# Performance work log

Measured on AMD Instinct MI355X. Metric: run time of the kernel, lower is better.

## Reference

```python
import jax, jax.numpy as jnp
import numpy as np

PRIME = 2147483647  # 2^31 - 1, MinHash modulus
GAMMA = 0.3
NUM_HEADS = 8


def minhash_sketch(ids, a, b):
    # ids: (B, L, S) int64 atom ids; a,b: (K,) hash coefficients
    # h[b,l,s,k] = (a[k]*id + b[k]) mod PRIME ; signature = min over the set axis S
    h = (ids[..., None] * a + b) % PRIME          # (B, L, S, K)
    return h.min(axis=2)                          # (B, L, K)


def jaccard_from_signatures(sig_q, sig_k):
    # sig_q: (B, Lq, K), sig_k: (B, Lk, K) -> (B, Lq, Lk) fraction of matching slots.
    # Scan over the K hash slots to avoid materializing a (B,Lq,Lk,K) tensor.
    B, Lq, K = sig_q.shape
    Lk = sig_k.shape[1]

    def step(acc, cols):
        qc, kc = cols                              # (B,Lq), (B,Lk)
        return acc + (qc[:, :, None] == kc[:, None, :]).astype(jnp.float32), None

    init = jnp.zeros((B, Lq, Lk), jnp.float32)
    xs = (jnp.moveaxis(sig_q, -1, 0), jnp.moveaxis(sig_k, -1, 0))
    acc, _ = jax.lax.scan(step, init, xs)
    return acc / K


def symdiff_from_jaccard(jacc, size_q, size_k):
    # |A ∩ B| = J/(1+J) * (|A|+|B|)  =>  |A Δ B| = (|A|+|B|) * (1-J)/(1+J)
    tot = size_q[:, :, None] + size_k[:, None, :]   # (B, Lq, Lk)
    return tot * (1.0 - jacc) / (1.0 + jacc)


def setup_inputs() -> dict:
    key = jax.random.key(0)
    ks = jax.random.split(key, 12)
    B, Lq, Lk, E, S, K, V = 4, 1024, 1024, 512, 8, 128, 32000
    w = lambda k: (jax.random.normal(k, (E, E), jnp.float32) * 0.02)
    return {
        "query": jax.random.normal(ks[0], (B, Lq, E), jnp.float32),
        "key": jax.random.normal(ks[1], (B, Lk, E), jnp.float32),
        "value": jax.random.normal(ks[2], (B, Lk, E), jnp.float32),
        "token_sets_q": jax.random.randint(ks[3], (B, Lq, S), 0, V).astype(jnp.int64),
        "token_sets_k": jax.random.randint(ks[4], (B, Lk, S), 0, V).astype(jnp.int64),
        "hash_a": jax.random.randint(ks[5], (K,), 1, PRIME - 1).astype(jnp.int64),
        "hash_b": jax.random.randint(ks[6], (K,), 0, PRIME - 1).astype(jnp.int64),
        "Wq": w(ks[7]), "bq": jnp.zeros((E,), jnp.float32),
        "Wk": w(ks[8]), "bk": jnp.zeros((E,), jnp.float32),
        "Wv": w(ks[9]), "bv": jnp.zeros((E,), jnp.float32),
        "Wo": w(ks[10]), "bo": jnp.zeros((E,), jnp.float32),
    }


def reference(query, key, value, token_sets_q, token_sets_k, hash_a, hash_b,
              Wq, bq, Wk, bk, Wv, bv, Wo, bo):
    B, Lq, E = query.shape
    Lk = key.shape[1]
    H = NUM_HEADS
    d = E // H

    # in-projections (torch Linear: x @ W^T + b); q,k are computed but the
    # attention scores come solely from the token-set kernel (gating disabled)
    q = query @ Wq.T + bq
    k = key @ Wk.T + bk
    v = (value @ Wv.T + bv).reshape(B, Lk, H, d).transpose(0, 2, 1, 3)  # (B,H,Lk,d)

    # MinHash sketches of per-token atom sets -> estimated Jaccard -> Δ-RBF score
    sig_q = minhash_sketch(token_sets_q, hash_a, hash_b)   # (B,Lq,K)
    sig_k = minhash_sketch(token_sets_k, hash_a, hash_b)   # (B,Lk,K)
    jacc = jaccard_from_signatures(sig_q, sig_k)           # (B,Lq,Lk)

    S = token_sets_q.shape[-1]
    size_q = jnp.full((B, Lq), S, jnp.float32)             # uniform CSR offsets -> |set| = S
    size_k = jnp.full((B, Lk), S, jnp.float32)
    delta = symdiff_from_jaccard(jacc, size_q, size_k)
    scores = jnp.exp(-GAMMA * delta)                       # (B,Lq,Lk), shared by all heads

    attn = jax.nn.softmax(scores, axis=-1)                 # no masks, no causal, dropout=0
    ctx = jnp.einsum('bqk,bhkd->bqhd', attn, v).reshape(B, Lq, E)
    return ctx @ Wo.T + bo
```

## Files before the change

kernel.cpp:

```cpp
#include <hip/hip_runtime.h>
#include <hip/hip_bf16.h>
#include <stdint.h>

#define PRIME 2147483647u
#define GAMMA 0.3f
#define K_HASH 128
#define S_SET 8
#define NB 4
#define LQ 1024
#define LK 1024
#define EDIM 512

typedef unsigned short ushort_t;
typedef __attribute__((ext_vector_type(8))) short short8;
typedef __attribute__((ext_vector_type(4))) float f32x4;

static __device__ __forceinline__ unsigned short f2bf(float f) {
    unsigned u = __builtin_bit_cast(unsigned, f);
    u += 0x7FFFu + ((u >> 16) & 1u);
    return (unsigned short)(u >> 16);
}

static __device__ __forceinline__ void glds16(const void* g, void* l) {
    __builtin_amdgcn_global_load_lds(
        (const __attribute__((address_space(1))) unsigned int*)g,
        (__attribute__((address_space(3))) unsigned int*)l, 16, 0, 0);
}

#define SWZ(r) ((((r) >> 2) & 3) ^ ((r) & 3))

static __device__ __forceinline__ unsigned nm2(unsigned acc, unsigned a,
                                               unsigned b, unsigned ones) {
    unsigned x = a ^ b, t;
    asm("v_pk_min_u16 %0, %1, %2" : "=v"(t) : "v"(x), "v"(ones));
    return acc + t;
}
static __device__ __forceinline__ unsigned nm8(unsigned acc, int4 q, int4 k,
                                               unsigned ones) {
    acc = nm2(acc, (unsigned)q.x, (unsigned)k.x, ones);
    acc = nm2(acc, (unsigned)q.y, (unsigned)k.y, ones);
    acc = nm2(acc, (unsigned)q.z, (unsigned)k.z, ones);
    acc = nm2(acc, (unsigned)q.w, (unsigned)k.w, ones);
    return acc;
}

#define CVT_N0 (NB * LK * EDIM)
#define CVT_N1 (EDIM * EDIM)
#define CVT_N2 (EDIM * EDIM)
#define CVT_BLOCKS ((CVT_N0 + CVT_N1 + CVT_N2) / (256 * 8))
#define SIG_BLOCKS (NB * (LQ + LK) / 2)

__global__ __launch_bounds__(256) void prep_kernel(
        const float* __restrict__ v, const float* __restrict__ wv,
        const float* __restrict__ wo,
        ushort_t* __restrict__ vb, ushort_t* __restrict__ wvb,
        ushort_t* __restrict__ wob,
        const int* __restrict__ ts_q, const int* __restrict__ ts_k,
        const int* __restrict__ ha, const int* __restrict__ hb,
        ushort_t* __restrict__ sig_q, ushort_t* __restrict__ sig_k,
        float* __restrict__ rs) {
    int blk = blockIdx.x;
    if (blk < CVT_BLOCKS) {
        size_t i = ((size_t)blk * 256 + threadIdx.x) * 8;
        const float* src; ushort_t* dst; size_t off;
        if (i < CVT_N0)                { src = v;  dst = vb;  off = i; }
        else if (i < CVT_N0 + CVT_N1)  { src = wv; dst = wvb; off = i - CVT_N0; }
        else                           { src = wo; dst = wob; off = i - CVT_N0 - CVT_N1; }
        float4 a = *(const float4*)(src + off);
        float4 b = *(const float4*)(src + off + 4);
        ushort4 o0, o1;
        o0.x = f2bf(a.x); o0.y = f2bf(a.y); o0.z = f2bf(a.z); o0.w = f2bf(a.w);
        o1.x = f2bf(b.x); o1.y = f2bf(b.y); o1.z = f2bf(b.z); o1.w = f2bf(b.w);
        *(ushort4*)(dst + off)     = o0;
        *(ushort4*)(dst + off + 4) = o1;
        return;
    }
    int sb = blk - CVT_BLOCKS;
    if (sb < 16) rs[sb * 256 + threadIdx.x] = 0.f;
    int half = threadIdx.x >> 7, k = threadIdx.x & 127;
    int row = sb * 2 + half;
    const int* ts = (row < NB * LQ) ? ts_q : ts_k;
    ushort_t* sig = (row < NB * LQ) ? sig_q : sig_k;
    int idx = row & (NB * LQ - 1);
    unsigned long long a  = (unsigned)ha[k];
    unsigned long long bb = (unsigned)hb[k];
    __shared__ int ids[2][S_SET];
    if (k < S_SET) ids[half][k] = ts[idx * S_SET + k];
    __syncthreads();
    unsigned mn = 0xFFFFFFFFu;
    #pragma unroll
    for (int s = 0; s < S_SET; s++) {
        unsigned long long x = a * (unsigned long long)(unsigned)ids[half][s] + bb;
        x = (x & PRIME) + (x >> 31);
        x = (x & PRIME) + (x >> 31);
        unsigned r = (unsigned)x;
        if (r >= PRIME) r -= PRIME;
        mn = (r < mn) ? r : mn;
    }
    sig[idx * K_HASH + k] = (ushort_t)mn;
}

__global__ __launch_bounds__(256) void jaccard_kernel(
        const ushort_t* __restrict__ sig_q, const ushort_t* __restrict__ sig_k,
        ushort_t* __restrict__ P, float* __restrict__ rs) {
    __shared__ int Qs[4][128 * 16];
    __shared__ int Ks[4][64 * 17];
    __shared__ float lut[K_HASH + 1];
    int tid = threadIdx.x;
    if (tid <= K_HASH) {
        float r = (float)(K_HASH - tid) / (float)(K_HASH + tid);
        lut[tid] = expf(expf(-GAMMA * (2.0f * S_SET) * r));
    }
    int b = blockIdx.z;
    int q0 = blockIdx.y * 128, j0 = blockIdx.x * 64;
    const int4* gq = (const int4*)(sig_q + ((size_t)b * LQ + q0) * K_HASH);
    const int4* gk = (const int4*)(sig_k + ((size_t)b * LK + j0) * K_HASH);
    int r0 = tid >> 2, g0 = tid & 3;
    int r1 = 64 + r0;
    #pragma unroll
    for (int ch = 0; ch < 4; ch++) {
        *(int4*)&Qs[ch][r0 * 16 + ((g0 + (r0 >> 3)) & 3) * 4] = gq[r0 * 16 + ch * 4 + g0];
        *(int4*)&Qs[ch][r1 * 16 + ((g0 + (r1 >> 3)) & 3) * 4] = gq[r1 * 16 + ch * 4 + g0];
        *(int4*)&Ks[ch][r0 * 17 + ((g0 + (r0 >> 5)) & 3) * 4] = gk[r0 * 16 + ch * 4 + g0];
    }
    __syncthreads();
    int tx = tid & 15, ty = tid >> 4;
    unsigned ones = 0x00010001u;
    unsigned acc[8][4] = {};

    auto ldq = [&](int ch, int cc, int4* qd) {
        #pragma unroll
        for (int i = 0; i < 8; i++)
            qd[i] = *(const int4*)&Qs[ch][(ty * 8 + i) * 16 + ((cc + ty) & 3) * 4];
    };
    auto ldk = [&](int ch, int cc, int4* kd) {
        #pragma unroll
        for (int j = 0; j < 4; j++)
            kd[j] = *(const int4*)&Ks[ch][(tx * 4 + j) * 17 + ((cc + (tx >> 3)) & 3) * 4];
    };

    int4 qa[8], ka[4], qb[8], kb[4];
    ldq(0, 0, qa); ldk(0, 0, ka);
    #pragma unroll 1
    for (int ch = 0; ch < 4; ch++) {
        #pragma unroll
        for (int cc = 0; cc < 4; cc++) {
            int nch = (cc == 3) ? ((ch + 1) & 3) : ch;
            int ncc = (cc + 1) & 3;
            ldq(nch, ncc, qb); ldk(nch, ncc, kb);
            #pragma unroll
            for (int i = 0; i < 8; i++)
                #pragma unroll
                for (int j = 0; j < 4; j++)
                    acc[i][j] = nm8(acc[i][j], qa[i], ka[j], ones);
            #pragma unroll
            for (int i = 0; i < 8; i++) qa[i] = qb[i];
            #pragma unroll
            for (int j = 0; j < 4; j++) ka[j] = kb[j];
        }
    }
    ushort_t* Pb = P + (size_t)b * LQ * LK;
    float fsum[8];
    #pragma unroll
    for (int i = 0; i < 8; i++) {
        ushort4 o;
        unsigned nm0 = (acc[i][0] & 0xFFFFu) + (acc[i][0] >> 16);
        unsigned nm1 = (acc[i][1] & 0xFFFFu) + (acc[i][1] >> 16);
        unsigned nm2_ = (acc[i][2] & 0xFFFFu) + (acc[i][2] >> 16);
        unsigned nm3 = (acc[i][3] & 0xFFFFu) + (acc[i][3] >> 16);
        float p0 = lut[K_HASH - nm0], p1 = lut[K_HASH - nm1];
        float p2 = lut[K_HASH - nm2_], p3 = lut[K_HASH - nm3];
        fsum[i] = (p0 + p1) + (p2 + p3);
        o.x = f2bf(p0); o.y = f2bf(p1); o.z = f2bf(p2); o.w = f2bf(p3);
        int row = q0 + ty * 8 + i;
        *(ushort4*)&Pb[(size_t)row * LK + j0 + tx * 4] = o;
    }
    __syncthreads();
    float* fs = (float*)&Qs[0][0];
    #pragma unroll
    for (int i = 0; i < 8; i++) fs[(ty * 8 + i) * 16 + tx] = fsum[i];
    __syncthreads();
    if (tid < 128) {
        float s = 0.f;
        #pragma unroll
        for (int t = 0; t < 16; t++) s += fs[tid * 16 + t];
        atomicAdd(&rs[(size_t)b * LQ + q0 + tid], s);
    }
}

#define EPI_ROWBIAS  0
#define EPI_ROWDIV   1
#define EPI_COLBIAS  2

template<int OUTF32, int MODE>
__global__ __launch_bounds__(256) void btgemm_kernel(
        const ushort_t* __restrict__ A, const ushort_t* __restrict__ B,
        void* __restrict__ C,
        const float* __restrict__ bias, const float* __restrict__ scale,
        int lda, int ldb, int ldc, int Kd,
        long long sA, long long sB, long long sC, long long sS) {
    __shared__ ushort_t As[2][64 * 32];
    __shared__ ushort_t Bs[2][64 * 32];
    int z = blockIdx.z;
    int m0 = blockIdx.y * 64, n0 = blockIdx.x * 64;
    int tid = threadIdx.x;
    int w = tid >> 6, lane = tid & 63;
    int wm = (w & 1) * 32, wn = (w >> 1) * 32;
    int mrow = lane & 15, kg = lane >> 4;

    int r = tid >> 2, c = (tid & 3) ^ SWZ(r);
    const ushort_t* pa = A + (size_t)z * sA + (size_t)(m0 + r) * lda + c * 8;
    const ushort_t* pb = B + (size_t)z * sB + (size_t)(n0 + r) * ldb + c * 8;

    int aoff[2], boff[2];
    #pragma unroll
    for (int s = 0; s < 2; s++) {
        int Ra = wm + s * 16 + mrow;
        aoff[s] = Ra * 32 + (kg ^ SWZ(Ra)) * 8;
        int Rb = wn + s * 16 + mrow;
        boff[s] = Rb * 32 + (kg ^ SWZ(Rb)) * 8;
    }

    f32x4 acc[2][2] = {};
    int nK = Kd >> 5;
    glds16(pa, &As[0][tid * 8]);
    glds16(pb, &Bs[0][tid * 8]);
    for (int i = 0; i < nK; i++) {
        __syncthreads();
        int cur = i & 1, nxt = cur ^ 1;
        if (i + 1 < nK) {
            int k0 = (i + 1) << 5;
            glds16(pa + k0, &As[nxt][tid * 8]);
            glds16(pb + k0, &Bs[nxt][tid * 8]);
        }
        short8 af[2], bh[2];
        #pragma unroll
        for (int s = 0; s < 2; s++) {
            af[s] = *(const short8*)&As[cur][aoff[s]];
            bh[s] = *(const short8*)&Bs[cur][boff[s]];
        }
        #pragma unroll
        for (int ii = 0; ii < 2; ii++)
            #pragma unroll
            for (int jj = 0; jj < 2; jj++)
                acc[ii][jj] = __builtin_amdgcn_mfma_f32_16x16x32_bf16(
                                  af[ii], bh[jj], acc[ii][jj], 0, 0, 0);
    }

    const float* sc = scale + (size_t)z * sS;
    int col = lane & 15, rbase = (lane >> 4) * 4;
    #pragma unroll
    for (int ii = 0; ii < 2; ii++) {
        #pragma unroll
        for (int jj = 0; jj < 2; jj++) {
            #pragma unroll
            for (int rr = 0; rr < 4; rr++) {
                int gm = m0 + wm + ii * 16 + rbase + rr;
                int gn = n0 + wn + jj * 16 + col;
                float v = acc[ii][jj][rr];
                if (MODE == EPI_ROWBIAS)     v += bias[gm];
                else if (MODE == EPI_ROWDIV) v /= sc[gm];
                else                         v += bias[gn];
                size_t cix = (size_t)z * sC + (size_t)gm * ldc + gn;
                if (OUTF32) ((float*)C)[cix] = v;
                else        ((ushort_t*)C)[cix] = f2bf(v);
            }
        }
    }
}

extern "C" void kernel_launch(void* const* d_in, const int* in_sizes, int n_in,
                              void* d_out, int out_size, void* d_ws, size_t ws_size,
                              hipStream_t stream) {
    const float* value = (const float*)d_in[2];
    const int* tsq = (const int*)d_in[3];
    const int* tsk = (const int*)d_in[4];
    const int* ha  = (const int*)d_in[5];
    const int* hb  = (const int*)d_in[6];
    const float* Wv = (const float*)d_in[11];
    const float* bv = (const float*)d_in[12];
    const float* Wo = (const float*)d_in[13];
    const float* bo = (const float*)d_in[14];
    float* out = (float*)d_out;

    char* ws = (char*)d_ws;
    ushort_t* sigq   = (ushort_t*)(ws);
    ushort_t* sigk   = (ushort_t*)(ws + (1ull << 20));
    ushort_t* P      = (ushort_t*)(ws + (4ull << 20));
    float* rs        = (float*)(ws + (12ull << 20));
    ushort_t* Vt     = (ushort_t*)(ws + (12ull << 20) + (1ull << 16));
    ushort_t* ctx    = (ushort_t*)(ws + (17ull << 20));
    ushort_t* Vb     = (ushort_t*)(ws + (21ull << 20));
    ushort_t* Wvb    = (ushort_t*)(ws + (25ull << 20));
    ushort_t* Wob    = (ushort_t*)(ws + (25ull << 20) + (512ull << 10));

    prep_kernel<<<CVT_BLOCKS + SIG_BLOCKS, 256, 0, stream>>>(
        value, Wv, Wo, Vb, Wvb, Wob, tsq, tsk, ha, hb, sigq, sigk, rs);

    jaccard_kernel<<<dim3(LK / 64, LQ / 128, NB), 256, 0, stream>>>(sigq, sigk, P, rs);

    btgemm_kernel<0, EPI_ROWBIAS><<<dim3(4096 / 64, 512 / 64, 1), 256, 0, stream>>>(
        Wvb, Vb, Vt, bv, rs ,
        EDIM, EDIM, NB * LK, EDIM, 0LL, 0LL, 0LL, 0LL);

    btgemm_kernel<0, EPI_ROWDIV><<<dim3(EDIM / 64, LQ / 64, NB), 256, 0, stream>>>(
        P, Vt, ctx, bv , rs,
        LK, NB * LK, EDIM, LK,
        (long long)LQ * LK, (long long)LK, (long long)LQ * EDIM, (long long)LQ);

    btgemm_kernel<1, EPI_COLBIAS><<<dim3(EDIM / 64, NB * LQ / 64, 1), 256, 0, stream>>>(
        ctx, Wob, out, bo, rs ,
        EDIM, EDIM, EDIM, EDIM, 0LL, 0LL, 0LL, 0LL);
}
```

Measured before the change: 156.6 us.

## Shrink Jaccard tile to 64x64 and stage signatures in two halves

The Jaccard kernel's output tile drops from 128x64 to 64x64, so each thread accumulates 4x4 instead of 8x4 counts and the grid doubles. The signature slots are now loaded into shared memory in two halves with an XOR-swizzled, padded layout, replacing the full preload and the register double-buffered LDS reads. This cuts shared memory and register use to raise occupancy and block count, at the cost of less reuse per loaded signature, extra barriers, and no software prefetch overlap.

New measurement: 154.8 us. No clear change (-1.1%).

```diff
diff --git a/kernel.cpp b/kernel.cpp
--- a/kernel.cpp
+++ b/kernel.cpp
@@ -103,8 +103,8 @@
 __global__ __launch_bounds__(256) void jaccard_kernel(
         const ushort_t* __restrict__ sig_q, const ushort_t* __restrict__ sig_k,
         ushort_t* __restrict__ P, float* __restrict__ rs) {
-    __shared__ int Qs[4][128 * 16];
-    __shared__ int Ks[4][64 * 17];
+    __shared__ int Qs[64 * 36];
+    __shared__ int Ks[64 * 36];
     __shared__ float lut[K_HASH + 1];
     int tid = threadIdx.x;
     if (tid <= K_HASH) {
@@ -112,75 +112,62 @@
         lut[tid] = expf(expf(-GAMMA * (2.0f * S_SET) * r));
     }
     int b = blockIdx.z;
-    int q0 = blockIdx.y * 128, j0 = blockIdx.x * 64;
+    int q0 = blockIdx.y * 64, j0 = blockIdx.x * 64;
     const int4* gq = (const int4*)(sig_q + ((size_t)b * LQ + q0) * K_HASH);
     const int4* gk = (const int4*)(sig_k + ((size_t)b * LK + j0) * K_HASH);
-    int r0 = tid >> 2, g0 = tid & 3;
-    int r1 = 64 + r0;
-    #pragma unroll
-    for (int ch = 0; ch < 4; ch++) {
-        *(int4*)&Qs[ch][r0 * 16 + ((g0 + (r0 >> 3)) & 3) * 4] = gq[r0 * 16 + ch * 4 + g0];
-        *(int4*)&Qs[ch][r1 * 16 + ((g0 + (r1 >> 3)) & 3) * 4] = gq[r1 * 16 + ch * 4 + g0];
-        *(int4*)&Ks[ch][r0 * 17 + ((g0 + (r0 >> 5)) & 3) * 4] = gk[r0 * 16 + ch * 4 + g0];
-    }
-    __syncthreads();
     int tx = tid & 15, ty = tid >> 4;
     unsigned ones = 0x00010001u;
-    unsigned acc[8][4] = {};
-
-    auto ldq = [&](int ch, int cc, int4* qd) {
-        #pragma unroll
-        for (int i = 0; i < 8; i++)
-            qd[i] = *(const int4*)&Qs[ch][(ty * 8 + i) * 16 + ((cc + ty) & 3) * 4];
-    };
-    auto ldk = [&](int ch, int cc, int4* kd) {
-        #pragma unroll
-        for (int j = 0; j < 4; j++)
-            kd[j] = *(const int4*)&Ks[ch][(tx * 4 + j) * 17 + ((cc + (tx >> 3)) & 3) * 4];
-    };
-
-    int4 qa[8], ka[4], qb[8], kb[4];
-    ldq(0, 0, qa); ldk(0, 0, ka);
+    unsigned acc[4][4] = {};
+    int sr = tid >> 2, sg0 = (tid & 3) * 2;
     #pragma unroll 1
-    for (int ch = 0; ch < 4; ch++) {
-        #pragma unroll
-        for (int cc = 0; cc < 4; cc++) {
-            int nch = (cc == 3) ? ((ch + 1) & 3) : ch;
-            int ncc = (cc + 1) & 3;
-            ldq(nch, ncc, qb); ldk(nch, ncc, kb);
-            #pragma unroll
-            for (int i = 0; i < 8; i++)
+    for (int h = 0; h < 2; h++) {
+        __syncthreads();
+        #pragma unroll
+        for (int u = 0; u < 2; u++) {
+            int g = sg0 + u;
+            *(int4*)&Qs[sr * 36 + ((g ^ (sr >> 2)) & 7) * 4] = gq[sr * 16 + h * 8 + g];
+            *(int4*)&Ks[sr * 36 + ((g ^ (sr >> 2)) & 7) * 4] = gk[sr * 16 + h * 8 + g];
+        }
+        __syncthreads();
+        #pragma unroll
+        for (int g = 0; g < 8; g++) {
+            int qx = ((g ^ ty) & 7) * 4, kx = ((g ^ tx) & 7) * 4;
+            int4 qv[4], kv[4];
+            #pragma unroll
+            for (int i = 0; i < 4; i++)
+                qv[i] = *(const int4*)&Qs[(ty * 4 + i) * 36 + qx];
+            #pragma unroll
+            for (int j = 0; j < 4; j++)
+                kv[j] = *(const int4*)&Ks[(tx * 4 + j) * 36 + kx];
+            #pragma unroll
+            for (int i = 0; i < 4; i++)
                 #pragma unroll
                 for (int j = 0; j < 4; j++)
-                    acc[i][j] = nm8(acc[i][j], qa[i], ka[j], ones);
-            #pragma unroll
-            for (int i = 0; i < 8; i++) qa[i] = qb[i];
-            #pragma unroll
-            for (int j = 0; j < 4; j++) ka[j] = kb[j];
+                    acc[i][j] = nm8(acc[i][j], qv[i], kv[j], ones);
         }
     }
     ushort_t* Pb = P + (size_t)b * LQ * LK;
-    float fsum[8];
-    #pragma unroll
-    for (int i = 0; i < 8; i++) {
+    float fsum[4];
+    #pragma unroll
+    for (int i = 0; i < 4; i++) {
         ushort4 o;
-        unsigned nm0 = (acc[i][0] & 0xFFFFu) + (acc[i][0] >> 16);
-        unsigned nm1 = (acc[i][1] & 0xFFFFu) + (acc[i][1] >> 16);
-        unsigned nm2_ = (acc[i][2] & 0xFFFFu) + (acc[i][2] >> 16);
-        unsigned nm3 = (acc[i][3] & 0xFFFFu) + (acc[i][3] >> 16);
-        float p0 = lut[K_HASH - nm0], p1 = lut[K_HASH - nm1];
-        float p2 = lut[K_HASH - nm2_], p3 = lut[K_HASH - nm3];
+        unsigned n0_ = (acc[i][0] & 0xFFFFu) + (acc[i][0] >> 16);
+        unsigned n1_ = (acc[i][1] & 0xFFFFu) + (acc[i][1] >> 16);
+        unsigned n2_ = (acc[i][2] & 0xFFFFu) + (acc[i][2] >> 16);
+        unsigned n3_ = (acc[i][3] & 0xFFFFu) + (acc[i][3] >> 16);
+        float p0 = lut[K_HASH - n0_], p1 = lut[K_HASH - n1_];
+        float p2 = lut[K_HASH - n2_], p3 = lut[K_HASH - n3_];
         fsum[i] = (p0 + p1) + (p2 + p3);
         o.x = f2bf(p0); o.y = f2bf(p1); o.z = f2bf(p2); o.w = f2bf(p3);
-        int row = q0 + ty * 8 + i;
+        int row = q0 + ty * 4 + i;
         *(ushort4*)&Pb[(size_t)row * LK + j0 + tx * 4] = o;
     }
     __syncthreads();
-    float* fs = (float*)&Qs[0][0];
-    #pragma unroll
-    for (int i = 0; i < 8; i++) fs[(ty * 8 + i) * 16 + tx] = fsum[i];
+    float* fs = (float*)&Qs[0];
+    #pragma unroll
+    for (int i = 0; i < 4; i++) fs[(ty * 4 + i) * 16 + tx] = fsum[i];
     __syncthreads();
-    if (tid < 128) {
+    if (tid < 64) {
         float s = 0.f;
         #pragma unroll
         for (int t = 0; t < 16; t++) s += fs[tid * 16 + t];
@@ -297,7 +284,7 @@
     prep_kernel<<<CVT_BLOCKS + SIG_BLOCKS, 256, 0, stream>>>(
         value, Wv, Wo, Vb, Wvb, Wob, tsq, tsk, ha, hb, sigq, sigk, rs);
 
-    jaccard_kernel<<<dim3(LK / 64, LQ / 128, NB), 256, 0, stream>>>(sigq, sigk, P, rs);
+    jaccard_kernel<<<dim3(LK / 64, LQ / 64, NB), 256, 0, stream>>>(sigq, sigk, P, rs);
 
     btgemm_kernel<0, EPI_ROWBIAS><<<dim3(4096 / 64, 512 / 64, 1), 256, 0, stream>>>(
         Wvb, Vb, Vt, bv, rs ,
```
